# Kernel tuning notes

Hardware: AMD Instinct MI355X
Metric: run time of the kernel (lower is better)

## Reference

```python
import jax, jax.numpy as jnp
import numpy as np

B, T = 8192, 26
V, E, H, L = 23, 100, 128, 64  # vocab, emb dim, GRU hidden, latent; LSTM hidden = E


def setup_inputs() -> dict:
    key = jax.random.key(0)
    ks = jax.random.split(key, 16)
    rn = lambda k, shape, scale=0.1: (jax.random.normal(k, shape, jnp.float32) * scale)
    emb = rn(ks[0], (V, E)).at[0].set(0.0)  # padding_idx=0 row zeroed
    return {
        "z": jax.random.normal(ks[1], (B, L), jnp.float32),
        "x_in": jax.random.randint(ks[2], (B, T), 0, V),
        "emb": emb,
        "fc_z_w": rn(ks[3], (H, L)), "fc_z_b": rn(ks[4], (H,)),
        "gru_wih": rn(ks[5], (3 * H, E)), "gru_whh": rn(ks[6], (3 * H, H)),
        "gru_bih": rn(ks[7], (3 * H,)), "gru_bhh": rn(ks[8], (3 * H,)),
        "lstm_wih": rn(ks[9], (4 * E, H)), "lstm_whh": rn(ks[10], (4 * E, E)),
        "lstm_bih": rn(ks[11], (4 * E,)), "lstm_bhh": rn(ks[12], (4 * E,)),
        "out_w": rn(ks[13], (V, E)), "out_b": rn(ks[14], (V,)),
    }


def _gru(e, h0, Wih, Whh, bih, bhh):
    # e: (B,T,E); precompute input projections for all steps, scan over T.
    xg = jnp.einsum('bti,gi->btg', e, Wih) + bih  # (B,T,3H)

    def step(h, x):
        hg = h @ Whh.T + bhh
        xr, xz, xn = jnp.split(x, 3, axis=-1)
        hr, hz, hn = jnp.split(hg, 3, axis=-1)
        r = jax.nn.sigmoid(xr + hr)
        zg = jax.nn.sigmoid(xz + hz)
        n = jnp.tanh(xn + r * hn)
        h_new = (1.0 - zg) * n + zg * h
        return h_new, h_new

    _, ys = jax.lax.scan(step, h0, jnp.swapaxes(xg, 0, 1))  # (T,B,H)
    return jnp.swapaxes(ys, 0, 1)


def _lstm(x, h0, c0, Wih, Whh, bih, bhh):
    xg = jnp.einsum('bti,gi->btg', x, Wih) + bih  # (B,T,4E)

    def step(hc, xt):
        h, c = hc
        g = xt + h @ Whh.T + bhh
        i, f, gg, o = jnp.split(g, 4, axis=-1)
        c_new = jax.nn.sigmoid(f) * c + jax.nn.sigmoid(i) * jnp.tanh(gg)
        h_new = jax.nn.sigmoid(o) * jnp.tanh(c_new)
        return (h_new, c_new), h_new

    _, ys = jax.lax.scan(step, (h0, c0), jnp.swapaxes(xg, 0, 1))
    return jnp.swapaxes(ys, 0, 1)


def reference(z, x_in, emb, fc_z_w, fc_z_b, gru_wih, gru_whh, gru_bih, gru_bhh,
              lstm_wih, lstm_whh, lstm_bih, lstm_bhh, out_w, out_b):
    h0 = jnp.tanh(z @ fc_z_w.T + fc_z_b)            # (B,H)
    e = emb[x_in]                                    # (B,T,E)
    y = _gru(e, h0, gru_wih, gru_whh, gru_bih, gru_bhh)           # (B,T,H)
    zeros = jnp.zeros((z.shape[0], E), dtype=z.dtype)
    y = _lstm(y, zeros, zeros, lstm_wih, lstm_whh, lstm_bih, lstm_bhh)  # (B,T,E)
    logits = jnp.einsum('bte,ve->btv', y, out_w) + out_b          # (B,T,V)
    return logits
```

## Files before the change

### kernel.cpp

```cpp
#include <hip/hip_runtime.h>
#include <stdint.h>
#include <stddef.h>

#define BB 8192
#define TT 26
#define VV 23
#define EE 100
#define HH 128
#define LL 64

typedef __attribute__((ext_vector_type(8))) short bf16x8;
typedef __attribute__((ext_vector_type(4))) float f32x4;

#define MFMA(a, b, c) __builtin_amdgcn_mfma_f32_16x16x32_bf16((a), (b), (c), 0, 0, 0)

#define OFF_GRUW   0ull
#define OFF_TBL    98304ull
#define OFF_LSTMW  122880ull
#define OFF_OUTW   352256ull
#define OFF_FCZW   360448ull
#define OFF_LBIAS  376832ull
#define OFF_Y      379904ull

__device__ __forceinline__ unsigned short f2bf(float f) {
  union { float f; unsigned u; } v; v.f = f;
  unsigned u = v.u;
  return (unsigned short)((u + 0x7FFFu + ((u >> 16) & 1u)) >> 16);
}
__device__ __forceinline__ unsigned short f2bf_fast(float f) {
  union { float f; unsigned u; } v; v.f = f;
  return (unsigned short)((v.u + 0x8000u) >> 16);
}
#define LOG2E 1.4426950408889634f
__device__ __forceinline__ float sigm(float x) {
  return __builtin_amdgcn_rcpf(1.0f + __builtin_amdgcn_exp2f(-x * LOG2E));
}
__device__ __forceinline__ float tanh_(float x) {
  return __builtin_fmaf(-2.0f,
      __builtin_amdgcn_rcpf(1.0f + __builtin_amdgcn_exp2f(x * (2.0f * LOG2E))), 1.0f);
}

__global__ __launch_bounds__(256) void prep_kernel(
    const float* __restrict__ emb, const float* __restrict__ fc_z_w,
    const float* __restrict__ gru_wih, const float* __restrict__ gru_whh,
    const float* __restrict__ gru_bih,
    const float* __restrict__ lstm_wih, const float* __restrict__ lstm_whh,
    const float* __restrict__ lstm_bih, const float* __restrict__ lstm_bhh,
    const float* __restrict__ out_w,
    char* __restrict__ ws)
{
  int e = blockIdx.x * 256 + threadIdx.x;

  if (e < 49152) {
    int j = e & 7, lane = (e >> 3) & 63, kc = (e >> 9) & 3, ct = e >> 11;
    int n = ct * 16 + (lane & 15);
    int k = kc * 32 + ((lane >> 4) & 3) * 8 + j;
    *(unsigned short*)(ws + OFF_GRUW + (size_t)e * 2) = f2bf(gru_whh[n * HH + k]);
    return;
  }
  e -= 49152;
  if (e < 12288) {
    int j = e & 7, lane = (e >> 3) & 63, ct = e >> 9;
    int n = ct * 16 + (lane & 15);
    int k = ((lane >> 4) & 3) * 8 + j;
    float v = 0.0f;
    if (k < VV) {
      float s0 = 0.f, s1 = 0.f, s2 = 0.f, s3 = 0.f;
      const float* ep = emb + k * EE;
      const float* wp = gru_wih + n * EE;
#pragma unroll 5
      for (int m = 0; m < EE; m += 4) {
        s0 += ep[m] * wp[m];     s1 += ep[m + 1] * wp[m + 1];
        s2 += ep[m + 2] * wp[m + 2]; s3 += ep[m + 3] * wp[m + 3];
      }
      v = gru_bih[n] + ((s0 + s1) + (s2 + s3));
    }
    *(unsigned short*)(ws + OFF_TBL + (size_t)e * 2) = f2bf(v);
    return;
  }
  e -= 12288;
  if (e < 114688) {
    int j = e & 7, lane = (e >> 3) & 63, kc = (e >> 9) & 7, ct = e >> 12;
    int row = ct * 16 + (lane & 15);
    int g = row / 112, c = row % 112;
    int q = (lane >> 4) & 3;
    float v = 0.0f;
    if (c < EE) {
      if (kc < 4) {
        int k = kc * 32 + q * 8 + j;
        v = lstm_wih[(g * EE + c) * HH + k];
      } else {
        int k = (kc - 4) * 32 + q * 8 + j;
        if (k < EE) v = lstm_whh[(g * EE + c) * EE + k];
      }
    }
    *(unsigned short*)(ws + OFF_LSTMW + (size_t)e * 2) = f2bf(v);
    return;
  }
  e -= 114688;
  if (e < 4096) {
    int j = e & 7, lane = (e >> 3) & 63, kc = (e >> 9) & 3, ct = e >> 11;
    int n = ct * 16 + (lane & 15);
    int k = kc * 32 + ((lane >> 4) & 3) * 8 + j;
    float v = (n < VV && k < EE) ? out_w[n * EE + k] : 0.0f;
    *(unsigned short*)(ws + OFF_OUTW + (size_t)e * 2) = f2bf(v);
    return;
  }
  e -= 4096;
  if (e < 8192) {
    int j = e & 7, lane = (e >> 3) & 63, kc = (e >> 9) & 1, ct = e >> 10;
    int n = ct * 16 + (lane & 15);
    int k = kc * 32 + ((lane >> 4) & 3) * 8 + j;
    *(unsigned short*)(ws + OFF_FCZW + (size_t)e * 2) = f2bf(fc_z_w[n * LL + k]);
    return;
  }
  e -= 8192;
  if (e < 448) {
    int g = e / 112, c = e % 112;
    float v = (c < EE) ? (lstm_bih[g * EE + c] + lstm_bhh[g * EE + c]) : 0.0f;
    *(float*)(ws + OFF_LBIAS + (size_t)e * 4) = v;
  }
}

__global__ __launch_bounds__(512, 4) void gru_kernel(
    const float* __restrict__ z, const int* __restrict__ x_in,
    const float* __restrict__ fc_z_b, const float* __restrict__ gru_bhh,
    char* __restrict__ ws)
{
  __shared__ unsigned short hfrag[2][2048];
  __shared__ unsigned char idx_lds[TT * 16];
  const int tid  = threadIdx.x;
  const int wv   = tid >> 6;
  const int lane = tid & 63;
  const int l15  = lane & 15;
  const int q    = (lane >> 4) & 3;
  const int blk  = blockIdx.x;

  for (int i = tid; i < TT * 16; i += 512) {
    int t = i >> 4, r = i & 15;
    idx_lds[i] = (unsigned char)x_in[(blk * 16 + r) * TT + t];
  }

  bf16x8 gw[3][4], tw[3];
#pragma unroll
  for (int g = 0; g < 3; g++) {
    int ct = g * 8 + wv;
#pragma unroll
    for (int kc = 0; kc < 4; kc++)
      gw[g][kc] = *(const bf16x8*)(ws + OFF_GRUW + (size_t)(ct * 4 + kc) * 1024 + lane * 16);
    tw[g] = *(const bf16x8*)(ws + OFF_TBL + (size_t)ct * 1024 + lane * 16);
  }
  const int col = wv * 16 + l15;
  const float b_r = gru_bhh[0 * HH + col];
  const float b_z = gru_bhh[1 * HH + col];
  const float b_n = gru_bhh[2 * HH + col];
  const int wbase = (col >> 5) * 512 + ((col >> 3) & 3) * 128 + (col & 7);

  float h[4];
  {
    bf16x8 fw0 = *(const bf16x8*)(ws + OFF_FCZW + (size_t)(wv * 2 + 0) * 1024 + lane * 16);
    bf16x8 fw1 = *(const bf16x8*)(ws + OFF_FCZW + (size_t)(wv * 2 + 1) * 1024 + lane * 16);
    const float* zp = z + (size_t)(blk * 16 + l15) * LL + q * 8;
    f32x4 z0 = *(const f32x4*)(zp);
    f32x4 z1 = *(const f32x4*)(zp + 4);
    f32x4 z2 = *(const f32x4*)(zp + 32);
    f32x4 z3 = *(const f32x4*)(zp + 36);
    bf16x8 za0, za1;
#pragma unroll
    for (int j = 0; j < 4; j++) {
      za0[j]     = (short)f2bf(z0[j]);
      za0[4 + j] = (short)f2bf(z1[j]);
      za1[j]     = (short)f2bf(z2[j]);
      za1[4 + j] = (short)f2bf(z3[j]);
    }
    float fzb = fc_z_b[col];
    f32x4 acc = {fzb, fzb, fzb, fzb};
    acc = MFMA(za0, fw0, acc);
    acc = MFMA(za1, fw1, acc);
#pragma unroll
    for (int i = 0; i < 4; i++) {
      h[i] = tanh_(acc[i]);
      hfrag[0][wbase + (q * 4 + i) * 8] = f2bf_fast(h[i]);
    }
  }
  __syncthreads();

  int cur = 0;
  for (int t = 0; t < TT; t++) {
    int iv = idx_lds[t * 16 + l15];
    bf16x8 oh;
#pragma unroll
    for (int j = 0; j < 8; j++)
      oh[j] = (short)((iv == q * 8 + j) ? 0x3F80 : 0);

    f32x4 ar  = {b_r, b_r, b_r, b_r};
    f32x4 az  = {b_z, b_z, b_z, b_z};
    f32x4 ahn = {b_n, b_n, b_n, b_n};
    f32x4 axn = {0.0f, 0.0f, 0.0f, 0.0f};
    ar  = MFMA(oh, tw[0], ar);
    az  = MFMA(oh, tw[1], az);
    axn = MFMA(oh, tw[2], axn);

    bf16x8 a[4];
#pragma unroll
    for (int kc = 0; kc < 4; kc++)
      a[kc] = *(const bf16x8*)((const char*)hfrag[cur] + kc * 1024 + lane * 16);
#pragma unroll
    for (int kc = 0; kc < 4; kc++) {
      ar  = MFMA(a[kc], gw[0][kc], ar);
      az  = MFMA(a[kc], gw[1][kc], az);
      ahn = MFMA(a[kc], gw[2][kc], ahn);
    }

    int nb = cur ^ 1;
#pragma unroll
    for (int i = 0; i < 4; i++) {
      float r  = sigm(ar[i]);
      float zg = sigm(az[i]);
      float n  = tanh_(__builtin_fmaf(r, ahn[i], axn[i]));
      h[i] = __builtin_fmaf(zg, h[i] - n, n);
      hfrag[nb][wbase + (q * 4 + i) * 8] = f2bf_fast(h[i]);
    }
    __syncthreads();
    if (wv < 4) {
      bf16x8 yv = *(const bf16x8*)((const char*)hfrag[nb] + wv * 1024 + lane * 16);
      *(bf16x8*)(ws + OFF_Y + ((size_t)(blk * TT + t) * 4 + wv) * 1024 + lane * 16) = yv;
    }
    cur = nb;
  }
}

__global__ __launch_bounds__(960) void lstm_kernel(
    const float* __restrict__ out_b, char* __restrict__ ws,
    float* __restrict__ out)
{
  __shared__ float Pbuf[2][4 * 7 * 64 * 4];
  __shared__ unsigned short hbuf[2][2048];
  const int tid  = threadIdx.x;
  const int wv   = tid >> 6;
  const int lane = tid & 63;
  const int l15  = lane & 15;
  const int q    = (lane >> 4) & 3;
  const int blk  = blockIdx.x;

  for (int i = tid; i < 4096; i += 960)
    ((unsigned short*)hbuf)[i] = 0;
  __syncthreads();

  if (wv < 7) {
    bf16x8 lwy[4][4];
#pragma unroll
    for (int g = 0; g < 4; g++)
#pragma unroll
      for (int kc = 0; kc < 4; kc++)
        lwy[g][kc] = *(const bf16x8*)(ws + OFF_LSTMW + (size_t)((g * 7 + wv) * 8 + kc) * 1024 + lane * 16);
    const int col = wv * 16 + l15;
    const float* lb = (const float*)(ws + OFF_LBIAS);
    float b[4];
#pragma unroll
    for (int g = 0; g < 4; g++) b[g] = lb[g * 112 + col];

    bf16x8 ya[4];
#pragma unroll
    for (int kc = 0; kc < 4; kc++)
      ya[kc] = *(const bf16x8*)(ws + OFF_Y + ((size_t)(blk * TT + 0) * 4 + kc) * 1024 + lane * 16);

    for (int p = 0; p < TT + 2; p++) {
      if (p <= TT - 1) {
#pragma unroll
        for (int g = 0; g < 4; g++) {
          f32x4 acc = {b[g], b[g], b[g], b[g]};
#pragma unroll
          for (int kc = 0; kc < 4; kc++)
            acc = MFMA(ya[kc], lwy[g][kc], acc);
          *(f32x4*)&Pbuf[p & 1][((g * 7 + wv) * 64 + lane) * 4] = acc;
        }
        if (p < TT - 1) {
#pragma unroll
          for (int kc = 0; kc < 4; kc++)
            ya[kc] = *(const bf16x8*)(ws + OFF_Y + ((size_t)(blk * TT + p + 1) * 4 + kc) * 1024 + lane * 16);
        }
      }
      __syncthreads();
    }
  } else if (wv < 14) {
    const int tile = wv - 7;
    bf16x8 lwh[4][4];
#pragma unroll
    for (int g = 0; g < 4; g++)
#pragma unroll
      for (int kc = 0; kc < 4; kc++)
        lwh[g][kc] = *(const bf16x8*)(ws + OFF_LSTMW + (size_t)((g * 7 + tile) * 8 + kc + 4) * 1024 + lane * 16);
    const int col = tile * 16 + l15;
    const int wbase = (col >> 5) * 512 + ((col >> 3) & 3) * 128 + (col & 7);
    float c[4] = {0, 0, 0, 0};

    for (int p = 0; p < TT + 2; p++) {
      if (p >= 1 && p <= TT) {
        const int rb = (p - 1) & 1;
        f32x4 ai = *(const f32x4*)&Pbuf[rb][((0 * 7 + tile) * 64 + lane) * 4];
        f32x4 af = *(const f32x4*)&Pbuf[rb][((1 * 7 + tile) * 64 + lane) * 4];
        f32x4 ag = *(const f32x4*)&Pbuf[rb][((2 * 7 + tile) * 64 + lane) * 4];
        f32x4 ao = *(const f32x4*)&Pbuf[rb][((3 * 7 + tile) * 64 + lane) * 4];
        bf16x8 ha[4];
#pragma unroll
        for (int kc = 0; kc < 4; kc++)
          ha[kc] = *(const bf16x8*)((const char*)hbuf[p & 1] + kc * 1024 + lane * 16);
#pragma unroll
        for (int kc = 0; kc < 4; kc++) {
          ai = MFMA(ha[kc], lwh[0][kc], ai);
          af = MFMA(ha[kc], lwh[1][kc], af);
          ag = MFMA(ha[kc], lwh[2][kc], ag);
          ao = MFMA(ha[kc], lwh[3][kc], ao);
        }
#pragma unroll
        for (int i = 0; i < 4; i++) {
          float ii = sigm(ai[i]), ff = sigm(af[i]);
          float gg = tanh_(ag[i]), oo = sigm(ao[i]);
          float cn = __builtin_fmaf(ff, c[i], ii * gg);
          c[i] = cn;
          hbuf[rb][wbase + (q * 4 + i) * 8] = f2bf_fast(oo * tanh_(cn));
        }
      }
      __syncthreads();
    }
  } else {
    bf16x8 ow[2][4];
#pragma unroll
    for (int ct = 0; ct < 2; ct++)
#pragma unroll
      for (int kc = 0; kc < 4; kc++)
        ow[ct][kc] = *(const bf16x8*)(ws + OFF_OUTW + (size_t)(ct * 4 + kc) * 1024 + lane * 16);
    float ob[2];
#pragma unroll
    for (int ct = 0; ct < 2; ct++) {
      int cv = ct * 16 + l15;
      ob[ct] = (cv < VV) ? out_b[cv] : 0.0f;
    }

    for (int p = 0; p < TT + 2; p++) {
      if (p >= 2) {
        const int t = p - 2;
        bf16x8 ha[4];
#pragma unroll
        for (int kc = 0; kc < 4; kc++)
          ha[kc] = *(const bf16x8*)((const char*)hbuf[p & 1] + kc * 1024 + lane * 16);
#pragma unroll
        for (int ct = 0; ct < 2; ct++) {
          f32x4 acc = {ob[ct], ob[ct], ob[ct], ob[ct]};
#pragma unroll
          for (int kc = 0; kc < 4; kc++)
            acc = MFMA(ha[kc], ow[ct][kc], acc);
          int cv = ct * 16 + l15;
          if (cv < VV) {
#pragma unroll
            for (int i = 0; i < 4; i++) {
              int rowg = blk * 16 + q * 4 + i;
              out[((size_t)rowg * TT + t) * VV + cv] = acc[i];
            }
          }
        }
      }
      __syncthreads();
    }
  }
}

extern "C" void kernel_launch(void* const* d_in, const int* in_sizes, int n_in,
                              void* d_out, int out_size, void* d_ws, size_t ws_size,
                              hipStream_t stream) {
  (void)in_sizes; (void)n_in; (void)out_size; (void)ws_size;
  const float* z        = (const float*)d_in[0];
  const int*   x_in     = (const int*)  d_in[1];
  const float* emb      = (const float*)d_in[2];
  const float* fc_z_w   = (const float*)d_in[3];
  const float* fc_z_b   = (const float*)d_in[4];
  const float* gru_wih  = (const float*)d_in[5];
  const float* gru_whh  = (const float*)d_in[6];
  const float* gru_bih  = (const float*)d_in[7];
  const float* gru_bhh  = (const float*)d_in[8];
  const float* lstm_wih = (const float*)d_in[9];
  const float* lstm_whh = (const float*)d_in[10];
  const float* lstm_bih = (const float*)d_in[11];
  const float* lstm_bhh = (const float*)d_in[12];
  const float* out_w    = (const float*)d_in[13];
  const float* out_b    = (const float*)d_in[14];
  char*  ws  = (char*)d_ws;
  float* out = (float*)d_out;

  prep_kernel<<<738, 256, 0, stream>>>(emb, fc_z_w, gru_wih, gru_whh, gru_bih,
                                       lstm_wih, lstm_whh, lstm_bih, lstm_bhh,
                                       out_w, ws);
  gru_kernel<<<512, 512, 0, stream>>>(z, x_in, fc_z_b, gru_bhh, ws);
  lstm_kernel<<<512, 960, 0, stream>>>(out_b, ws, out);
}
```

Measured before the change: 190.6 us.

## Split logits projection out of LSTM kernel and defer GRU/LSTM output stores

```diff
diff --git a/kernel.cpp b/kernel.cpp
--- a/kernel.cpp
+++ b/kernel.cpp
@@ -21,6 +21,8 @@
 #define OFF_FCZW   360448ull
 #define OFF_LBIAS  376832ull
 #define OFF_Y      379904ull
+
+__device__ __forceinline__ void force_frag(bf16x8& v) { asm volatile("" : "+v"(v)); }
 
 __device__ __forceinline__ unsigned short f2bf(float f) {
   union { float f; unsigned u; } v; v.f = f;
@@ -125,7 +127,8 @@
 __global__ __launch_bounds__(512, 4) void gru_kernel(
     const float* __restrict__ z, const int* __restrict__ x_in,
     const float* __restrict__ fc_z_b, const float* __restrict__ gru_bhh,
-    char* __restrict__ ws)
+    const unsigned short* __restrict__ gruw, const unsigned short* __restrict__ tbl,
+    const unsigned short* __restrict__ fczw, unsigned short* __restrict__ yout)
 {
   __shared__ unsigned short hfrag[2][2048];
   __shared__ unsigned char idx_lds[TT * 16];
@@ -146,9 +149,12 @@
   for (int g = 0; g < 3; g++) {
     int ct = g * 8 + wv;
 #pragma unroll
-    for (int kc = 0; kc < 4; kc++)
-      gw[g][kc] = *(const bf16x8*)(ws + OFF_GRUW + (size_t)(ct * 4 + kc) * 1024 + lane * 16);
-    tw[g] = *(const bf16x8*)(ws + OFF_TBL + (size_t)ct * 1024 + lane * 16);
+    for (int kc = 0; kc < 4; kc++) {
+      gw[g][kc] = *(const bf16x8*)(gruw + (size_t)(ct * 4 + kc) * 512 + lane * 8);
+      force_frag(gw[g][kc]);
+    }
+    tw[g] = *(const bf16x8*)(tbl + (size_t)ct * 512 + lane * 8);
+    force_frag(tw[g]);
   }
   const int col = wv * 16 + l15;
   const float b_r = gru_bhh[0 * HH + col];
@@ -158,8 +164,8 @@
 
   float h[4];
   {
-    bf16x8 fw0 = *(const bf16x8*)(ws + OFF_FCZW + (size_t)(wv * 2 + 0) * 1024 + lane * 16);
-    bf16x8 fw1 = *(const bf16x8*)(ws + OFF_FCZW + (size_t)(wv * 2 + 1) * 1024 + lane * 16);
+    bf16x8 fw0 = *(const bf16x8*)(fczw + (size_t)(wv * 2 + 0) * 512 + lane * 8);
+    bf16x8 fw1 = *(const bf16x8*)(fczw + (size_t)(wv * 2 + 1) * 512 + lane * 8);
     const float* zp = z + (size_t)(blk * 16 + l15) * LL + q * 8;
     f32x4 z0 = *(const f32x4*)(zp);
     f32x4 z1 = *(const f32x4*)(zp + 4);
@@ -187,6 +193,10 @@
 
   int cur = 0;
   for (int t = 0; t < TT; t++) {
+    if (t > 0 && wv < 4) {
+      bf16x8 yv = *(const bf16x8*)((const char*)hfrag[cur] + wv * 1024 + lane * 16);
+      *(bf16x8*)(yout + ((size_t)(blk * TT + (t - 1)) * 4 + wv) * 512 + lane * 8) = yv;
+    }
     int iv = idx_lds[t * 16 + l15];
     bf16x8 oh;
 #pragma unroll
@@ -222,17 +232,17 @@
       hfrag[nb][wbase + (q * 4 + i) * 8] = f2bf_fast(h[i]);
     }
     __syncthreads();
-    if (wv < 4) {
-      bf16x8 yv = *(const bf16x8*)((const char*)hfrag[nb] + wv * 1024 + lane * 16);
-      *(bf16x8*)(ws + OFF_Y + ((size_t)(blk * TT + t) * 4 + wv) * 1024 + lane * 16) = yv;
-    }
     cur = nb;
   }
-}
-
-__global__ __launch_bounds__(960) void lstm_kernel(
-    const float* __restrict__ out_b, char* __restrict__ ws,
-    float* __restrict__ out)
+  if (wv < 4) {
+    bf16x8 yv = *(const bf16x8*)((const char*)hfrag[cur] + wv * 1024 + lane * 16);
+    *(bf16x8*)(yout + ((size_t)(blk * TT + (TT - 1)) * 4 + wv) * 512 + lane * 8) = yv;
+  }
+}
+
+__global__ __launch_bounds__(896, 4) void lstm_kernel(
+    const unsigned short* __restrict__ lstmw, const float* __restrict__ lbias,
+    unsigned short* __restrict__ ybuf)
 {
   __shared__ float Pbuf[2][4 * 7 * 64 * 4];
   __shared__ unsigned short hbuf[2][2048];
@@ -243,7 +253,7 @@
   const int q    = (lane >> 4) & 3;
   const int blk  = blockIdx.x;
 
-  for (int i = tid; i < 4096; i += 960)
+  for (int i = tid; i < 4096; i += 896)
     ((unsigned short*)hbuf)[i] = 0;
   __syncthreads();
 
@@ -252,20 +262,25 @@
 #pragma unroll
     for (int g = 0; g < 4; g++)
 #pragma unroll
-      for (int kc = 0; kc < 4; kc++)
-        lwy[g][kc] = *(const bf16x8*)(ws + OFF_LSTMW + (size_t)((g * 7 + wv) * 8 + kc) * 1024 + lane * 16);
+      for (int kc = 0; kc < 4; kc++) {
+        lwy[g][kc] = *(const bf16x8*)(lstmw + (size_t)((g * 7 + wv) * 8 + kc) * 512 + lane * 8);
+        force_frag(lwy[g][kc]);
+      }
     const int col = wv * 16 + l15;
-    const float* lb = (const float*)(ws + OFF_LBIAS);
     float b[4];
 #pragma unroll
-    for (int g = 0; g < 4; g++) b[g] = lb[g * 112 + col];
+    for (int g = 0; g < 4; g++) b[g] = lbias[g * 112 + col];
 
     bf16x8 ya[4];
 #pragma unroll
     for (int kc = 0; kc < 4; kc++)
-      ya[kc] = *(const bf16x8*)(ws + OFF_Y + ((size_t)(blk * TT + 0) * 4 + kc) * 1024 + lane * 16);
+      ya[kc] = *(const bf16x8*)(ybuf + ((size_t)(blk * TT + 0) * 4 + kc) * 512 + lane * 8);
 
     for (int p = 0; p < TT + 2; p++) {
+      if (p >= 2 && wv < 4) {
+        bf16x8 hv = *(const bf16x8*)((const char*)hbuf[p & 1] + wv * 1024 + lane * 16);
+        *(bf16x8*)(ybuf + ((size_t)(blk * TT + (p - 2)) * 4 + wv) * 512 + lane * 8) = hv;
+      }
       if (p <= TT - 1) {
 #pragma unroll
         for (int g = 0; g < 4; g++) {
@@ -278,19 +293,21 @@
         if (p < TT - 1) {
 #pragma unroll
           for (int kc = 0; kc < 4; kc++)
-            ya[kc] = *(const bf16x8*)(ws + OFF_Y + ((size_t)(blk * TT + p + 1) * 4 + kc) * 1024 + lane * 16);
+            ya[kc] = *(const bf16x8*)(ybuf + ((size_t)(blk * TT + p + 1) * 4 + kc) * 512 + lane * 8);
         }
       }
       __syncthreads();
     }
-  } else if (wv < 14) {
+  } else {
     const int tile = wv - 7;
     bf16x8 lwh[4][4];
 #pragma unroll
     for (int g = 0; g < 4; g++)
 #pragma unroll
-      for (int kc = 0; kc < 4; kc++)
-        lwh[g][kc] = *(const bf16x8*)(ws + OFF_LSTMW + (size_t)((g * 7 + tile) * 8 + kc + 4) * 1024 + lane * 16);
+      for (int kc = 0; kc < 4; kc++) {
+        lwh[g][kc] = *(const bf16x8*)(lstmw + (size_t)((g * 7 + tile) * 8 + kc + 4) * 512 + lane * 8);
+        force_frag(lwh[g][kc]);
+      }
     const int col = tile * 16 + l15;
     const int wbase = (col >> 5) * 512 + ((col >> 3) & 3) * 128 + (col & 7);
     float c[4] = {0, 0, 0, 0};
@@ -324,44 +341,54 @@
       }
       __syncthreads();
     }
-  } else {
-    bf16x8 ow[2][4];
-#pragma unroll
-    for (int ct = 0; ct < 2; ct++)
+  }
+}
+
+__global__ __launch_bounds__(512) void logits_kernel(
+    const float* __restrict__ out_b, const unsigned short* __restrict__ hg,
+    const unsigned short* __restrict__ outw, float* __restrict__ out)
+{
+  const int tid  = threadIdx.x;
+  const int wv   = tid >> 6;
+  const int lane = tid & 63;
+  const int l15  = lane & 15;
+  const int q    = (lane >> 4) & 3;
+  const int blk  = blockIdx.x;
+
+  bf16x8 ow[2][4];
+#pragma unroll
+  for (int ct = 0; ct < 2; ct++)
+#pragma unroll
+    for (int kc = 0; kc < 4; kc++) {
+      ow[ct][kc] = *(const bf16x8*)(outw + (size_t)(ct * 4 + kc) * 512 + lane * 8);
+      force_frag(ow[ct][kc]);
+    }
+  float ob[2];
+#pragma unroll
+  for (int ct = 0; ct < 2; ct++) {
+    int cv = ct * 16 + l15;
+    ob[ct] = (cv < VV) ? out_b[cv] : 0.0f;
+  }
+
+  for (int t = wv; t < TT; t += 8) {
+    bf16x8 ha[4];
+#pragma unroll
+    for (int kc = 0; kc < 4; kc++)
+      ha[kc] = *(const bf16x8*)(hg + ((size_t)(blk * TT + t) * 4 + kc) * 512 + lane * 8);
+#pragma unroll
+    for (int ct = 0; ct < 2; ct++) {
+      f32x4 acc = {ob[ct], ob[ct], ob[ct], ob[ct]};
 #pragma unroll
       for (int kc = 0; kc < 4; kc++)
-        ow[ct][kc] = *(const bf16x8*)(ws + OFF_OUTW + (size_t)(ct * 4 + kc) * 1024 + lane * 16);
-    float ob[2];
-#pragma unroll
-    for (int ct = 0; ct < 2; ct++) {
+        acc = MFMA(ha[kc], ow[ct][kc], acc);
       int cv = ct * 16 + l15;
-      ob[ct] = (cv < VV) ? out_b[cv] : 0.0f;
-    }
-
-    for (int p = 0; p < TT + 2; p++) {
-      if (p >= 2) {
-        const int t = p - 2;
-        bf16x8 ha[4];
-#pragma unroll
-        for (int kc = 0; kc < 4; kc++)
-          ha[kc] = *(const bf16x8*)((const char*)hbuf[p & 1] + kc * 1024 + lane * 16);
-#pragma unroll
-        for (int ct = 0; ct < 2; ct++) {
-          f32x4 acc = {ob[ct], ob[ct], ob[ct], ob[ct]};
-#pragma unroll
-          for (int kc = 0; kc < 4; kc++)
-            acc = MFMA(ha[kc], ow[ct][kc], acc);
-          int cv = ct * 16 + l15;
-          if (cv < VV) {
-#pragma unroll
-            for (int i = 0; i < 4; i++) {
-              int rowg = blk * 16 + q * 4 + i;
-              out[((size_t)rowg * TT + t) * VV + cv] = acc[i];
-            }
-          }
+      if (cv < VV) {
+#pragma unroll
+        for (int i = 0; i < 4; i++) {
+          int rowg = blk * 16 + q * 4 + i;
+          out[((size_t)rowg * TT + t) * VV + cv] = acc[i];
         }
       }
-      __syncthreads();
     }
   }
 }
@@ -388,9 +415,19 @@
   char*  ws  = (char*)d_ws;
   float* out = (float*)d_out;
 
+  const unsigned short* gruw  = (const unsigned short*)(ws + OFF_GRUW);
+  const unsigned short* tblp  = (const unsigned short*)(ws + OFF_TBL);
+  const unsigned short* lstmw = (const unsigned short*)(ws + OFF_LSTMW);
+  const unsigned short* outw  = (const unsigned short*)(ws + OFF_OUTW);
+  const unsigned short* fczw  = (const unsigned short*)(ws + OFF_FCZW);
+  const float*          lbias = (const float*)(ws + OFF_LBIAS);
+  unsigned short*       ybuf  = (unsigned short*)(ws + OFF_Y);
+
   prep_kernel<<<738, 256, 0, stream>>>(emb, fc_z_w, gru_wih, gru_whh, gru_bih,
                                        lstm_wih, lstm_whh, lstm_bih, lstm_bhh,
                                        out_w, ws);
-  gru_kernel<<<512, 512, 0, stream>>>(z, x_in, fc_z_b, gru_bhh, ws);
-  lstm_kernel<<<512, 960, 0, stream>>>(out_b, ws, out);
-}
+  gru_kernel<<<512, 512, 0, stream>>>(z, x_in, fc_z_b, gru_bhh,
+                                      gruw, tblp, fczw, ybuf);
+  lstm_kernel<<<512, 896, 0, stream>>>(lstmw, lbias, ybuf);
+  logits_kernel<<<512, 512, 0, stream>>>(out_b, ybuf, outw, out);
+}
```

Result: slower. 209.2 us (+9.8%).
